# Kernel optimization log

Measured on AMD Instinct MI355X. Metric: run time of the kernel, lower is better.

The kernel has to match this reference:

```python
import jax, jax.numpy as jnp
import numpy as np


def setup_inputs() -> dict:
    key = jax.random.key(0)
    B, T = 4096, 2048
    # small positive strains keep C = 2E + I symmetric positive definite
    strain = jax.random.uniform(key, (B, T, 3), dtype=jnp.float32) * 0.2
    ki0 = jnp.float32(1.5)  # learned exponent for order-0 stretch term
    ki1 = jnp.float32(1.0)  # scale on log(J) term (init 1.0 in torch code)
    return {"strain": strain, "ki0": ki0, "ki1": ki1}


def reference(strain, ki0, ki1):
    # Build symmetric 2x2 right Cauchy-Green tensor C = 2E + I implicitly:
    # E00 = s0, E11 = s1, E01 = E10 = 0.5*s2  ->  C01 = s2
    c00 = 2.0 * strain[..., 0] + 1.0          # [B, T]
    c11 = 2.0 * strain[..., 1] + 1.0
    c01 = strain[..., 2]

    det = c00 * c11 - c01 * c01               # det(C)
    J = jnp.sqrt(det)
    log_J = jnp.log(J)

    # closed-form eigenvalues of symmetric 2x2, ascending (matches eigvalsh)
    mean = 0.5 * (c00 + c11)
    rad = jnp.sqrt(0.25 * (c00 - c11) ** 2 + c01 * c01)
    sq_eig = jnp.stack([mean - rad, mean + rad], axis=-1)  # [B, T, 2]

    eig = jnp.sqrt(sq_eig)                    # principal stretches
    aux = J ** (-1.0 / 3.0)                   # volumetric regularizer
    reg_eig = eig * aux[..., None]            # [B, T, 2]

    # order_stretches = 1: one powered-stretch block + scaled log(J)
    kan_input = jnp.concatenate(
        [reg_eig ** ki0, (log_J * ki1)[..., None]], axis=-1
    )                                         # [B, T, 3]
    return kan_input
```

## Files before the change

kernel.cpp:

```cpp
#include <hip/hip_runtime.h>


typedef unsigned int u32;

#define WAVE_LDS_FENCE() asm volatile("s_waitcnt lgkmcnt(0)" ::: "memory")

__device__ __forceinline__ void compute3(float s0, float s1, float s2,
                                         float ki0, float ki1,
                                         float& o0, float& o1, float& o2) {
    const float c00 = __builtin_fmaf(2.0f, s0, 1.0f);
    const float c11 = __builtin_fmaf(2.0f, s1, 1.0f);
    const float c01 = s2;
    const float det = c00 * c11 - c01 * c01;
    const float l2det = __builtin_log2f(det);
    const float mean = 0.5f * (c00 + c11);
    const float diff = 0.5f * (c00 - c11);
    const float rad  = __builtin_sqrtf(__builtin_fmaf(diff, diff, c01 * c01));
    const float l2lam0 = __builtin_log2f(mean - rad);
    const float l2a = -0.16666666667f * l2det;
    o0 = __builtin_exp2f(ki0 * __builtin_fmaf(0.5f, l2lam0, l2a));
    o1 = __builtin_exp2f(ki0 * __builtin_fmaf(-0.5f, l2lam0,
                                  __builtin_fmaf(0.5f, l2det, l2a)));
    o2 = (0.34657359028f * l2det) * ki1;
}

constexpr int TPB = 256;
constexpr int WPB = TPB / 64;
constexpr int WCH = 192;
constexpr int BCH = WPB * WCH;

__global__ __launch_bounds__(TPB) void kan_v9_wavelds(
    const float* __restrict__ strain,
    const float* __restrict__ ki0p,
    const float* __restrict__ ki1p,
    float* __restrict__ out,
    int nfloat_i)
{
    __shared__ float4 slab[WPB][WCH];
    const float ki0 = ki0p[0];
    const float ki1 = ki1p[0];
    const u32 nfloat = (u32)nfloat_i;
    const u32 nf4 = nfloat >> 2;
    const u32 nchunk = nf4 / BCH;
    const u32 t = threadIdx.x;
    const u32 w = t >> 6;
    const u32 l = t & 63u;
    float4* S = slab[w];
    const float4* __restrict__ in4 = (const float4*)strain;
    float4* __restrict__ out4 = (float4*)out;
    const u32 G = gridDim.x;

    u32 c = blockIdx.x;
    float4 p0, p1, p2;
    if (c < nchunk) {
        const float4* b = in4 + (size_t)c * BCH + w * WCH;
        p0 = b[l]; p1 = b[l + 64]; p2 = b[l + 128];
    }
    while (c < nchunk) {
        S[l] = p0; S[l + 64] = p1; S[l + 128] = p2;

        const u32 cn = c + G;
        if (cn < nchunk) {
            const float4* b = in4 + (size_t)cn * BCH + w * WCH;
            p0 = b[l]; p1 = b[l + 64]; p2 = b[l + 128];
        }

        WAVE_LDS_FENCE();

        const float4 a  = S[3u * l];
        const float4 b4 = S[3u * l + 1];
        const float4 c4 = S[3u * l + 2];

        float o0,o1,o2,o3,o4,o5,o6,o7,o8,o9,oa,ob;
        compute3(a.x,  a.y,  a.z,  ki0, ki1, o0, o1, o2);
        compute3(a.w,  b4.x, b4.y, ki0, ki1, o3, o4, o5);
        compute3(b4.z, b4.w, c4.x, ki0, ki1, o6, o7, o8);
        compute3(c4.y, c4.z, c4.w, ki0, ki1, o9, oa, ob);

        S[3u * l]     = make_float4(o0, o1, o2, o3);
        S[3u * l + 1] = make_float4(o4, o5, o6, o7);
        S[3u * l + 2] = make_float4(o8, o9, oa, ob);

        WAVE_LDS_FENCE();

        const float4 q0 = S[l], q1 = S[l + 64], q2 = S[l + 128];
        float4* ob4 = out4 + (size_t)c * BCH + w * WCH;
        ob4[l] = q0; ob4[l + 64] = q1; ob4[l + 128] = q2;

        WAVE_LDS_FENCE();

        c = cn;
    }

    const u32 ntrip = nfloat / 3u;
    const u32 t0 = nchunk * (BCH * 4u / 3u);
    const u32 gs = G * (u32)TPB;
    for (u32 e = t0 + blockIdx.x * (u32)TPB + t; e < ntrip; e += gs) {
        float x0, x1, x2;
        compute3(strain[3 * e], strain[3 * e + 1], strain[3 * e + 2],
                 ki0, ki1, x0, x1, x2);
        out[3 * e]     = x0;
        out[3 * e + 1] = x1;
        out[3 * e + 2] = x2;
    }
}

extern "C" void kernel_launch(void* const* d_in, const int* in_sizes, int n_in,
                              void* d_out, int out_size, void* d_ws, size_t ws_size,
                              hipStream_t stream) {
    const float* strain = (const float*)d_in[0];
    const float* ki0p   = (const float*)d_in[1];
    const float* ki1p   = (const float*)d_in[2];
    float* out = (float*)d_out;

    const int nfloat = in_sizes[0];
    const u32 nf4 = ((u32)nfloat) >> 2;
    u32 blocks = nf4 / (u32)BCH;
    if (blocks > 2048u) blocks = 2048u;
    if (blocks < 1u) blocks = 1u;

    kan_v9_wavelds<<<(int)blocks, TPB, 0, stream>>>(strain, ki0p, ki1p, out, nfloat);
}
```

Before: 179.5 us.

## Double-buffer chunk prefetch two iterations ahead with nontemporal stores and fewer blocks

Prefetches input two chunks ahead using two register sets, so more global loads are in flight per wave. Output stores become nontemporal, and the trailing LDS fence is dropped. The grid shrinks to at most 1024 blocks (nchunk/8), so each block handles more chunks. This adds register pressure. Dropping the fence after the final LDS read relies on the next LDS write being ordered correctly.

```diff
diff --git a/kernel.cpp b/kernel.cpp
--- a/kernel.cpp
+++ b/kernel.cpp
@@ -2,6 +2,7 @@
 
 
 typedef unsigned int u32;
+typedef float f32x4 __attribute__((ext_vector_type(4)));
 
 #define WAVE_LDS_FENCE() asm volatile("s_waitcnt lgkmcnt(0)" ::: "memory")
 
@@ -29,7 +30,7 @@
 constexpr int WCH = 192;
 constexpr int BCH = WPB * WCH;
 
-__global__ __launch_bounds__(TPB) void kan_v9_wavelds(
+__global__ __launch_bounds__(TPB) void kan_v12_mlp(
     const float* __restrict__ strain,
     const float* __restrict__ ki0p,
     const float* __restrict__ ki1p,
@@ -40,8 +41,8 @@
     const float ki0 = ki0p[0];
     const float ki1 = ki1p[0];
     const u32 nfloat = (u32)nfloat_i;
-    const u32 nf4 = nfloat >> 2;
-    const u32 nchunk = nf4 / BCH;
+    const u32 nquads = nfloat >> 2;
+    const u32 nchunk = nquads / BCH;
     const u32 t = threadIdx.x;
     const u32 w = t >> 6;
     const u32 l = t & 63u;
@@ -50,32 +51,26 @@
     float4* __restrict__ out4 = (float4*)out;
     const u32 G = gridDim.x;
 
-    u32 c = blockIdx.x;
-    float4 p0, p1, p2;
-    if (c < nchunk) {
-        const float4* b = in4 + (size_t)c * BCH + w * WCH;
-        p0 = b[l]; p1 = b[l + 64]; p2 = b[l + 128];
-    }
-    while (c < nchunk) {
-        S[l] = p0; S[l + 64] = p1; S[l + 128] = p2;
+    auto do_chunk = [&](u32 cc, float4& r0, float4& r1, float4& r2) {
+        S[l] = r0; S[l + 64] = r1; S[l + 128] = r2;
 
-        const u32 cn = c + G;
-        if (cn < nchunk) {
-            const float4* b = in4 + (size_t)cn * BCH + w * WCH;
-            p0 = b[l]; p1 = b[l + 64]; p2 = b[l + 128];
+        const u32 cf = cc + 2u * G;
+        if (cf < nchunk) {
+            const float4* p = in4 + (size_t)cf * BCH + (size_t)w * WCH;
+            r0 = p[l]; r1 = p[l + 64]; r2 = p[l + 128];
         }
 
         WAVE_LDS_FENCE();
 
-        const float4 a  = S[3u * l];
-        const float4 b4 = S[3u * l + 1];
-        const float4 c4 = S[3u * l + 2];
+        const float4 x = S[3u * l];
+        const float4 y = S[3u * l + 1];
+        const float4 z = S[3u * l + 2];
 
         float o0,o1,o2,o3,o4,o5,o6,o7,o8,o9,oa,ob;
-        compute3(a.x,  a.y,  a.z,  ki0, ki1, o0, o1, o2);
-        compute3(a.w,  b4.x, b4.y, ki0, ki1, o3, o4, o5);
-        compute3(b4.z, b4.w, c4.x, ki0, ki1, o6, o7, o8);
-        compute3(c4.y, c4.z, c4.w, ki0, ki1, o9, oa, ob);
+        compute3(x.x, x.y, x.z, ki0, ki1, o0, o1, o2);
+        compute3(x.w, y.x, y.y, ki0, ki1, o3, o4, o5);
+        compute3(y.z, y.w, z.x, ki0, ki1, o6, o7, o8);
+        compute3(z.y, z.z, z.w, ki0, ki1, o9, oa, ob);
 
         S[3u * l]     = make_float4(o0, o1, o2, o3);
         S[3u * l + 1] = make_float4(o4, o5, o6, o7);
@@ -83,13 +78,27 @@
 
         WAVE_LDS_FENCE();
 
-        const float4 q0 = S[l], q1 = S[l + 64], q2 = S[l + 128];
-        float4* ob4 = out4 + (size_t)c * BCH + w * WCH;
-        ob4[l] = q0; ob4[l + 64] = q1; ob4[l + 128] = q2;
+        f32x4* d = (f32x4*)(out4 + (size_t)cc * BCH + (size_t)w * WCH);
+        __builtin_nontemporal_store(*(const f32x4*)&S[l],       d + l);
+        __builtin_nontemporal_store(*(const f32x4*)&S[l + 64],  d + l + 64);
+        __builtin_nontemporal_store(*(const f32x4*)&S[l + 128], d + l + 128);
+    };
 
-        WAVE_LDS_FENCE();
-
-        c = cn;
+    u32 c = blockIdx.x;
+    float4 a0, a1, a2, b0, b1, b2;
+    if (c < nchunk) {
+        const float4* p = in4 + (size_t)c * BCH + (size_t)w * WCH;
+        a0 = p[l]; a1 = p[l + 64]; a2 = p[l + 128];
+    }
+    if (c + G < nchunk) {
+        const float4* p = in4 + (size_t)(c + G) * BCH + (size_t)w * WCH;
+        b0 = p[l]; b1 = p[l + 64]; b2 = p[l + 128];
+    }
+    while (c < nchunk) {
+        do_chunk(c, a0, a1, a2);
+        const u32 cb = c + G;
+        if (cb < nchunk) do_chunk(cb, b0, b1, b2);
+        c += 2u * G;
     }
 
     const u32 ntrip = nfloat / 3u;
@@ -114,10 +123,11 @@
     float* out = (float*)d_out;
 
     const int nfloat = in_sizes[0];
-    const u32 nf4 = ((u32)nfloat) >> 2;
-    u32 blocks = nf4 / (u32)BCH;
-    if (blocks > 2048u) blocks = 2048u;
+    const u32 nquads = ((u32)nfloat) >> 2;
+    const u32 nchunk = nquads / (u32)BCH;
+    u32 blocks = nchunk / 8u;
+    if (blocks > 1024u) blocks = 1024u;
     if (blocks < 1u) blocks = 1u;
 
-    kan_v9_wavelds<<<(int)blocks, TPB, 0, stream>>>(strain, ki0p, ki1p, out, nfloat);
+    kan_v12_mlp<<<(int)blocks, TPB, 0, stream>>>(strain, ki0p, ki1p, out, nfloat);
 }
```

Measured after the change: 181.8 us. No clear change (+1.3%).

## Replace LDS-staged transpose with direct strided float4 loads, two triples per iteration

Applied to the files above, without the earlier changes.

Drops the per-wave LDS staging slab and its fences. Each thread now loads its three consecutive float4s straight from global memory, computes four triples and stores them back. The main loop handles two independent triple-groups per iteration so more loads are in flight. This trades fully coalesced global accesses for a 48-byte per-thread stride, which may waste memory transactions, in return for removing LDS traffic and synchronisation.

```diff
diff --git a/kernel.cpp b/kernel.cpp
--- a/kernel.cpp
+++ b/kernel.cpp
@@ -2,8 +2,6 @@
 
 
 typedef unsigned int u32;
-
-#define WAVE_LDS_FENCE() asm volatile("s_waitcnt lgkmcnt(0)" ::: "memory")
 
 __device__ __forceinline__ void compute3(float s0, float s1, float s2,
                                          float ki0, float ki1,
@@ -24,77 +22,70 @@
     o2 = (0.34657359028f * l2det) * ki1;
 }
 
+__device__ __forceinline__ void do_triple(const float4* __restrict__ in4,
+                                          float4* __restrict__ out4,
+                                          u32 i, float ki0, float ki1) {
+    const float4 x = in4[3u * i];
+    const float4 y = in4[3u * i + 1];
+    const float4 z = in4[3u * i + 2];
+    float o0,o1,o2,o3,o4,o5,o6,o7,o8,o9,oa,ob;
+    compute3(x.x, x.y, x.z, ki0, ki1, o0, o1, o2);
+    compute3(x.w, y.x, y.y, ki0, ki1, o3, o4, o5);
+    compute3(y.z, y.w, z.x, ki0, ki1, o6, o7, o8);
+    compute3(z.y, z.z, z.w, ki0, ki1, o9, oa, ob);
+    out4[3u * i]     = make_float4(o0, o1, o2, o3);
+    out4[3u * i + 1] = make_float4(o4, o5, o6, o7);
+    out4[3u * i + 2] = make_float4(o8, o9, oa, ob);
+}
+
 constexpr int TPB = 256;
-constexpr int WPB = TPB / 64;
-constexpr int WCH = 192;
-constexpr int BCH = WPB * WCH;
 
-__global__ __launch_bounds__(TPB) void kan_v9_wavelds(
+__global__ __launch_bounds__(TPB) void kan_v13_direct(
     const float* __restrict__ strain,
     const float* __restrict__ ki0p,
     const float* __restrict__ ki1p,
     float* __restrict__ out,
     int nfloat_i)
 {
-    __shared__ float4 slab[WPB][WCH];
     const float ki0 = ki0p[0];
     const float ki1 = ki1p[0];
     const u32 nfloat = (u32)nfloat_i;
-    const u32 nf4 = nfloat >> 2;
-    const u32 nchunk = nf4 / BCH;
+    const u32 nquads = nfloat >> 2;
+    const u32 ntriple = nquads / 3u;
     const u32 t = threadIdx.x;
-    const u32 w = t >> 6;
-    const u32 l = t & 63u;
-    float4* S = slab[w];
     const float4* __restrict__ in4 = (const float4*)strain;
     float4* __restrict__ out4 = (float4*)out;
-    const u32 G = gridDim.x;
+    const u32 gs = gridDim.x * (u32)TPB;
 
-    u32 c = blockIdx.x;
-    float4 p0, p1, p2;
-    if (c < nchunk) {
-        const float4* b = in4 + (size_t)c * BCH + w * WCH;
-        p0 = b[l]; p1 = b[l + 64]; p2 = b[l + 128];
-    }
-    while (c < nchunk) {
-        S[l] = p0; S[l + 64] = p1; S[l + 128] = p2;
-
-        const u32 cn = c + G;
-        if (cn < nchunk) {
-            const float4* b = in4 + (size_t)cn * BCH + w * WCH;
-            p0 = b[l]; p1 = b[l + 64]; p2 = b[l + 128];
-        }
-
-        WAVE_LDS_FENCE();
-
-        const float4 a  = S[3u * l];
-        const float4 b4 = S[3u * l + 1];
-        const float4 c4 = S[3u * l + 2];
+    u32 iA = blockIdx.x * (u32)TPB + t;
+    for (; iA + gs < ntriple; iA += 2u * gs) {
+        const u32 iB = iA + gs;
+        const float4 ax = in4[3u * iA],     ay = in4[3u * iA + 1], az = in4[3u * iA + 2];
+        const float4 bx = in4[3u * iB],     by = in4[3u * iB + 1], bz = in4[3u * iB + 2];
 
         float o0,o1,o2,o3,o4,o5,o6,o7,o8,o9,oa,ob;
-        compute3(a.x,  a.y,  a.z,  ki0, ki1, o0, o1, o2);
-        compute3(a.w,  b4.x, b4.y, ki0, ki1, o3, o4, o5);
-        compute3(b4.z, b4.w, c4.x, ki0, ki1, o6, o7, o8);
-        compute3(c4.y, c4.z, c4.w, ki0, ki1, o9, oa, ob);
+        compute3(ax.x, ax.y, ax.z, ki0, ki1, o0, o1, o2);
+        compute3(ax.w, ay.x, ay.y, ki0, ki1, o3, o4, o5);
+        compute3(ay.z, ay.w, az.x, ki0, ki1, o6, o7, o8);
+        compute3(az.y, az.z, az.w, ki0, ki1, o9, oa, ob);
+        out4[3u * iA]     = make_float4(o0, o1, o2, o3);
+        out4[3u * iA + 1] = make_float4(o4, o5, o6, o7);
+        out4[3u * iA + 2] = make_float4(o8, o9, oa, ob);
 
-        S[3u * l]     = make_float4(o0, o1, o2, o3);
-        S[3u * l + 1] = make_float4(o4, o5, o6, o7);
-        S[3u * l + 2] = make_float4(o8, o9, oa, ob);
-
-        WAVE_LDS_FENCE();
-
-        const float4 q0 = S[l], q1 = S[l + 64], q2 = S[l + 128];
-        float4* ob4 = out4 + (size_t)c * BCH + w * WCH;
-        ob4[l] = q0; ob4[l + 64] = q1; ob4[l + 128] = q2;
-
-        WAVE_LDS_FENCE();
-
-        c = cn;
+        compute3(bx.x, bx.y, bx.z, ki0, ki1, o0, o1, o2);
+        compute3(bx.w, by.x, by.y, ki0, ki1, o3, o4, o5);
+        compute3(by.z, by.w, bz.x, ki0, ki1, o6, o7, o8);
+        compute3(bz.y, bz.z, bz.w, ki0, ki1, o9, oa, ob);
+        out4[3u * iB]     = make_float4(o0, o1, o2, o3);
+        out4[3u * iB + 1] = make_float4(o4, o5, o6, o7);
+        out4[3u * iB + 2] = make_float4(o8, o9, oa, ob);
+    }
+    for (; iA < ntriple; iA += gs) {
+        do_triple(in4, out4, iA, ki0, ki1);
     }
 
     const u32 ntrip = nfloat / 3u;
-    const u32 t0 = nchunk * (BCH * 4u / 3u);
-    const u32 gs = G * (u32)TPB;
+    const u32 t0 = ntriple * 4u;
     for (u32 e = t0 + blockIdx.x * (u32)TPB + t; e < ntrip; e += gs) {
         float x0, x1, x2;
         compute3(strain[3 * e], strain[3 * e + 1], strain[3 * e + 2],
@@ -114,10 +105,11 @@
     float* out = (float*)d_out;
 
     const int nfloat = in_sizes[0];
-    const u32 nf4 = ((u32)nfloat) >> 2;
-    u32 blocks = nf4 / (u32)BCH;
+    const u32 nquads = ((u32)nfloat) >> 2;
+    const u32 ntriple = nquads / 3u;
+    u32 blocks = (ntriple + (u32)TPB - 1u) / (u32)TPB;
     if (blocks > 2048u) blocks = 2048u;
     if (blocks < 1u) blocks = 1u;
 
-    kan_v9_wavelds<<<(int)blocks, TPB, 0, stream>>>(strain, ki0p, ki1p, out, nfloat);
+    kan_v13_direct<<<(int)blocks, TPB, 0, stream>>>(strain, ki0p, ki1p, out, nfloat);
 }
```

After: 185.2 us. +3.2%, slower.
